# Kernel tuning notes

Hardware: AMD Instinct MI355X
Metric: run time of the kernel (lower is better)

The kernel has to match this reference:

```python
import jax, jax.numpy as jnp
import numpy as np

B, L, E, H = 4, 1024, 256, 8
DH = E // H  # head_size = 32


def setup_inputs() -> dict:
    key = jax.random.key(0)
    ks = jax.random.split(key, 12)
    node_features = jax.random.normal(ks[0], (B, L, E), dtype=jnp.float32)
    # sparse-ish adjacency with self loops so no row is all-masked
    adj = jax.random.bernoulli(ks[1], 0.05, (B, L, L))
    adj = adj | jnp.eye(L, dtype=bool)[None]
    key_edge_features = jax.random.normal(ks[2], (B, L, L, DH), dtype=jnp.float32)
    s = 1.0 / np.sqrt(E)
    Wq = jax.random.normal(ks[3], (E, E), dtype=jnp.float32) * s
    bq = jnp.zeros((E,), dtype=jnp.float32)
    Wk = jax.random.normal(ks[4], (E, E), dtype=jnp.float32) * s
    bk = jnp.zeros((E,), dtype=jnp.float32)
    Wv = jax.random.normal(ks[5], (E, E), dtype=jnp.float32) * s
    bv = jnp.zeros((E,), dtype=jnp.float32)
    Wo = jax.random.normal(ks[6], (E, E), dtype=jnp.float32) * s
    bo = jnp.zeros((E,), dtype=jnp.float32)
    return {"node_features": node_features, "batched_adj": adj,
            "key_edge_features": key_edge_features,
            "Wq": Wq, "bq": bq, "Wk": Wk, "bk": bk,
            "Wv": Wv, "bv": bv, "Wo": Wo, "bo": bo}


def _heads(x):
    # (B, L, E) -> (B, H, L, DH)
    b, l, _ = x.shape
    return x.reshape(b, l, H, DH).transpose(0, 2, 1, 3)


def reference(node_features, batched_adj, key_edge_features,
              Wq, bq, Wk, bk, Wv, bv, Wo, bo):
    Q = _heads(node_features @ Wq.T + bq)  # (B,H,L,DH)
    K = _heads(node_features @ Wk.T + bk)
    V = _heads(node_features @ Wv.T + bv)
    scores = jnp.einsum('bhnd,bhmd->bhnm', Q, K)
    scores = scores + jnp.einsum('bhnd,bnmd->bhnm', Q, key_edge_features)
    scores = scores / jnp.sqrt(jnp.asarray(E, dtype=scores.dtype))
    adj = batched_adj[:, None, :, :]  # (B,1,L,L) broadcast over heads
    scores = jnp.where(adj, scores, -jnp.inf)
    probs = jax.nn.softmax(scores, axis=-1)
    probs = jnp.where(jnp.isnan(probs), 0.0, probs)  # rows with no edges -> 0
    out = jnp.einsum('bhnm,bhmd->bhnd', probs, V)  # (B,H,L,DH)
    out = out.transpose(0, 2, 1, 3).reshape(node_features.shape[0], -1, E)
    return out @ Wo.T + bo
```

## Files before the change

### kernel.cpp

```cpp
#include <hip/hip_runtime.h>

#define Bv 4
#define Lv 1024
#define Ev 256
#define Hv 8
#define DHv 32

__global__ __launch_bounds__(256) void gemm_fused(
    const float* __restrict__ A,
    const float* __restrict__ W0, const float* __restrict__ b0, float* __restrict__ C0,
    const float* __restrict__ W1, const float* __restrict__ b1, float* __restrict__ C1,
    const float* __restrict__ W2, const float* __restrict__ b2, float* __restrict__ C2) {
    __shared__ float Xs[32][34];
    __shared__ float Ws[32][68];
    const int g = blockIdx.y >> 2;
    const float* __restrict__ W    = (g == 0) ? W0 : (g == 1) ? W1 : W2;
    const float* __restrict__ bias = (g == 0) ? b0 : (g == 1) ? b1 : b2;
    float* __restrict__ C          = (g == 0) ? C0 : (g == 1) ? C1 : C2;

    const int row0 = blockIdx.x * 32;
    const int col0 = (blockIdx.y & 3) * 64;
    const int t = threadIdx.x;
    const int tx = t & 15, ty = t >> 4;
    const int lr = t >> 3, lk = (t & 7) * 4;

    float acc[2][4] = {};

    for (int k0 = 0; k0 < 256; k0 += 32) {
        const float4 av = *(const float4*)&A[(size_t)(row0 + lr) * 256 + k0 + lk];
        const float4 w0 = *(const float4*)&W[(size_t)(col0 + lr) * 256 + k0 + lk];
        const float4 w1 = *(const float4*)&W[(size_t)(col0 + 32 + lr) * 256 + k0 + lk];
        Xs[lk + 0][lr] = av.x; Xs[lk + 1][lr] = av.y;
        Xs[lk + 2][lr] = av.z; Xs[lk + 3][lr] = av.w;
        Ws[lk + 0][lr] = w0.x; Ws[lk + 1][lr] = w0.y;
        Ws[lk + 2][lr] = w0.z; Ws[lk + 3][lr] = w0.w;
        Ws[lk + 0][32 + lr] = w1.x; Ws[lk + 1][32 + lr] = w1.y;
        Ws[lk + 2][32 + lr] = w1.z; Ws[lk + 3][32 + lr] = w1.w;
        __syncthreads();

        #pragma unroll
        for (int kk = 0; kk < 32; ++kk) {
            const float2 a2 = *(const float2*)&Xs[kk][ty * 2];
            const float4 b4 = *(const float4*)&Ws[kk][tx * 4];
            acc[0][0] = fmaf(a2.x, b4.x, acc[0][0]);
            acc[0][1] = fmaf(a2.x, b4.y, acc[0][1]);
            acc[0][2] = fmaf(a2.x, b4.z, acc[0][2]);
            acc[0][3] = fmaf(a2.x, b4.w, acc[0][3]);
            acc[1][0] = fmaf(a2.y, b4.x, acc[1][0]);
            acc[1][1] = fmaf(a2.y, b4.y, acc[1][1]);
            acc[1][2] = fmaf(a2.y, b4.z, acc[1][2]);
            acc[1][3] = fmaf(a2.y, b4.w, acc[1][3]);
        }
        __syncthreads();
    }

    const float4 bv4 = *(const float4*)&bias[col0 + tx * 4];
    #pragma unroll
    for (int ri = 0; ri < 2; ++ri) {
        const int row = row0 + ty * 2 + ri;
        float4 o;
        o.x = acc[ri][0] + bv4.x; o.y = acc[ri][1] + bv4.y;
        o.z = acc[ri][2] + bv4.z; o.w = acc[ri][3] + bv4.w;
        *(float4*)&C[(size_t)row * 256 + col0 + tx * 4] = o;
    }
}

__global__ __launch_bounds__(256) void attn_sparse(const float* __restrict__ Qb,
                                                   const float* __restrict__ Kb,
                                                   const float* __restrict__ Vb,
                                                   const int* __restrict__ adj,
                                                   const float* __restrict__ KE,
                                                   float* __restrict__ AT) {
    __shared__ __align__(16) float Qs[Ev];
    __shared__ __align__(16) float S[Hv][260];
    __shared__ int idxm[256];
    __shared__ int cntS;
    __shared__ float mh[Hv], lh[Hv], scaleh[Hv];

    const int bid = blockIdx.x;
    const int b = bid >> 10;
    const int n = bid & 1023;
    const int t = threadIdx.x;
    const int lane = t & 63;
    const int h_of_t = t >> 5;
    const size_t nrow = (size_t)(b * Lv + n) * Lv;

    Qs[t] = Qb[(size_t)(b * Lv + n) * Ev + t] * 0.0625f;
    if (t < Hv) { mh[t] = -1e30f; lh[t] = 0.f; }

    float acc = 0.f;
    const float* __restrict__ vcol = Vb + (size_t)b * Lv * Ev + t;
    const float4* __restrict__ K4 = (const float4*)Kb;
    const float4* __restrict__ KE4 = (const float4*)KE;
    const float4* __restrict__ Q4 = (const float4*)Qs;

    for (int c = 0; c < 4; ++c) {
        if (t == 0) cntS = 0;
        __syncthreads();

        const int m = c * 256 + t;
        const bool p = adj[nrow + m] != 0;
        const unsigned long long mask = __ballot(p);
        const int prefix = __popcll(mask & ((1ull << lane) - 1ull));
        int base = 0;
        if (lane == 0) base = atomicAdd(&cntS, __popcll(mask));
        base = __shfl(base, 0, 64);
        if (p) idxm[base + prefix] = m;
        __syncthreads();

        const int cnt = cntS;

        for (int tb = 0; tb < cnt * 8; tb += 256) {
            const int task = tb + t;
            if (task < cnt * 8) {
                const int ei = task >> 3, h = task & 7;
                const int mm = idxm[ei];
                const float4* kp = K4 + (size_t)(b * Lv + mm) * 64 + h * 8;
                const float4* kep = KE4 + (nrow + mm) * 8;
                const float4* qp = Q4 + h * 8;
                float dot = 0.f;
                #pragma unroll
                for (int j = 0; j < 8; ++j) {
                    const float4 kv = kp[j], kf = kep[j], qv = qp[j];
                    dot = fmaf(qv.x, kv.x + kf.x, dot);
                    dot = fmaf(qv.y, kv.y + kf.y, dot);
                    dot = fmaf(qv.z, kv.z + kf.z, dot);
                    dot = fmaf(qv.w, kv.w + kf.w, dot);
                }
                S[h][ei] = dot;
            }
        }
        __syncthreads();

        {
            const int h = t >> 5, d = t & 31;
            float cmax = -1e30f;
            for (int i = d; i < cnt; i += 32) cmax = fmaxf(cmax, S[h][i]);
            #pragma unroll
            for (int off = 16; off >= 1; off >>= 1)
                cmax = fmaxf(cmax, __shfl_xor(cmax, off, 64));
            const float oldm = mh[h];
            const float newm = fmaxf(oldm, cmax);
            float csum = 0.f;
            for (int i = d; i < cnt; i += 32) {
                const float pz = __expf(S[h][i] - newm);
                S[h][i] = pz;
                csum += pz;
            }
            #pragma unroll
            for (int off = 16; off >= 1; off >>= 1)
                csum += __shfl_xor(csum, off, 64);
            if (d == 0) {
                const float sc = __expf(oldm - newm);
                scaleh[h] = sc;
                lh[h] = lh[h] * sc + csum;
                mh[h] = newm;
            }
        }
        __syncthreads();

        {
            acc *= scaleh[h_of_t];
            int i = 0;
            for (; i + 4 <= cnt; i += 4) {
                const int m0 = idxm[i], m1 = idxm[i + 1], m2 = idxm[i + 2], m3 = idxm[i + 3];
                const float p0 = S[h_of_t][i],     p1 = S[h_of_t][i + 1];
                const float p2 = S[h_of_t][i + 2], p3 = S[h_of_t][i + 3];
                const float v0 = vcol[(size_t)m0 * Ev];
                const float v1 = vcol[(size_t)m1 * Ev];
                const float v2 = vcol[(size_t)m2 * Ev];
                const float v3 = vcol[(size_t)m3 * Ev];
                acc = fmaf(p0, v0, acc);
                acc = fmaf(p1, v1, acc);
                acc = fmaf(p2, v2, acc);
                acc = fmaf(p3, v3, acc);
            }
            for (; i < cnt; ++i)
                acc = fmaf(S[h_of_t][i], vcol[(size_t)idxm[i] * Ev], acc);
        }
        __syncthreads();
    }

    AT[(size_t)(b * Lv + n) * Ev + t] = acc / lh[h_of_t];
}

extern "C" void kernel_launch(void* const* d_in, const int* in_sizes, int n_in,
                              void* d_out, int out_size, void* d_ws, size_t ws_size,
                              hipStream_t stream) {
    const float* X   = (const float*)d_in[0];
    const int*   adj = (const int*)d_in[1];
    const float* KE  = (const float*)d_in[2];
    const float* Wq  = (const float*)d_in[3];
    const float* bq  = (const float*)d_in[4];
    const float* Wk  = (const float*)d_in[5];
    const float* bk  = (const float*)d_in[6];
    const float* Wv  = (const float*)d_in[7];
    const float* bv  = (const float*)d_in[8];
    const float* Wo  = (const float*)d_in[9];
    const float* bo  = (const float*)d_in[10];

    const size_t NE = (size_t)Bv * Lv * Ev;
    float* Qb = (float*)d_ws;
    float* Kb = Qb + NE;
    float* Vb = Kb + NE;
    float* AT = Vb + NE;
    float* out = (float*)d_out;

    const dim3 blk(256);

    hipLaunchKernelGGL(gemm_fused, dim3(128, 12), blk, 0, stream, X,
                       Wq, bq, Qb, Wk, bk, Kb, Wv, bv, Vb);
    hipLaunchKernelGGL(attn_sparse, dim3(Bv * Lv), blk, 0, stream,
                       Qb, Kb, Vb, adj, KE, AT);
    hipLaunchKernelGGL(gemm_fused, dim3(128, 4), blk, 0, stream, AT,
                       Wo, bo, out, Wo, bo, out, Wo, bo, out);
}
```

Before: 723.4 us.

## Compact adjacency once per row and enlarge GEMM tiles to 64x64

The attention kernel now compacts all four 256-column chunks of the adjacency row into one index list up front, then processes the nonzeros in chunks of 128. This replaces four chunk passes, each running a softmax update and several barriers, with roughly one or two passes at this sparsity. The projection GEMM tile grows from 32x64 to 64x64 with a 4x4 register micro-tile, which halves the block count and raises arithmetic per shared-memory load. In exchange the GEMM uses more registers and runs fewer blocks per launch.

```diff
diff --git a/kernel.cpp b/kernel.cpp
--- a/kernel.cpp
+++ b/kernel.cpp
@@ -5,59 +5,59 @@
 #define Ev 256
 #define Hv 8
 #define DHv 32
+#define CH 128
 
 __global__ __launch_bounds__(256) void gemm_fused(
     const float* __restrict__ A,
     const float* __restrict__ W0, const float* __restrict__ b0, float* __restrict__ C0,
     const float* __restrict__ W1, const float* __restrict__ b1, float* __restrict__ C1,
     const float* __restrict__ W2, const float* __restrict__ b2, float* __restrict__ C2) {
-    __shared__ float Xs[32][34];
+    __shared__ float Xs[32][68];
     __shared__ float Ws[32][68];
     const int g = blockIdx.y >> 2;
     const float* __restrict__ W    = (g == 0) ? W0 : (g == 1) ? W1 : W2;
     const float* __restrict__ bias = (g == 0) ? b0 : (g == 1) ? b1 : b2;
     float* __restrict__ C          = (g == 0) ? C0 : (g == 1) ? C1 : C2;
 
-    const int row0 = blockIdx.x * 32;
+    const int row0 = blockIdx.x * 64;
     const int col0 = (blockIdx.y & 3) * 64;
     const int t = threadIdx.x;
     const int tx = t & 15, ty = t >> 4;
-    const int lr = t >> 3, lk = (t & 7) * 4;
-
-    float acc[2][4] = {};
+    const int lr = t >> 2;
+    const int lk = (t & 3) * 8;
+
+    float acc[4][4] = {};
 
     for (int k0 = 0; k0 < 256; k0 += 32) {
-        const float4 av = *(const float4*)&A[(size_t)(row0 + lr) * 256 + k0 + lk];
+        const float4 a0 = *(const float4*)&A[(size_t)(row0 + lr) * 256 + k0 + lk];
+        const float4 a1 = *(const float4*)&A[(size_t)(row0 + lr) * 256 + k0 + lk + 4];
         const float4 w0 = *(const float4*)&W[(size_t)(col0 + lr) * 256 + k0 + lk];
-        const float4 w1 = *(const float4*)&W[(size_t)(col0 + 32 + lr) * 256 + k0 + lk];
-        Xs[lk + 0][lr] = av.x; Xs[lk + 1][lr] = av.y;
-        Xs[lk + 2][lr] = av.z; Xs[lk + 3][lr] = av.w;
-        Ws[lk + 0][lr] = w0.x; Ws[lk + 1][lr] = w0.y;
-        Ws[lk + 2][lr] = w0.z; Ws[lk + 3][lr] = w0.w;
-        Ws[lk + 0][32 + lr] = w1.x; Ws[lk + 1][32 + lr] = w1.y;
-        Ws[lk + 2][32 + lr] = w1.z; Ws[lk + 3][32 + lr] = w1.w;
+        const float4 w1 = *(const float4*)&W[(size_t)(col0 + lr) * 256 + k0 + lk + 4];
+        Xs[lk + 0][lr] = a0.x; Xs[lk + 1][lr] = a0.y; Xs[lk + 2][lr] = a0.z; Xs[lk + 3][lr] = a0.w;
+        Xs[lk + 4][lr] = a1.x; Xs[lk + 5][lr] = a1.y; Xs[lk + 6][lr] = a1.z; Xs[lk + 7][lr] = a1.w;
+        Ws[lk + 0][lr] = w0.x; Ws[lk + 1][lr] = w0.y; Ws[lk + 2][lr] = w0.z; Ws[lk + 3][lr] = w0.w;
+        Ws[lk + 4][lr] = w1.x; Ws[lk + 5][lr] = w1.y; Ws[lk + 6][lr] = w1.z; Ws[lk + 7][lr] = w1.w;
         __syncthreads();
 
         #pragma unroll
         for (int kk = 0; kk < 32; ++kk) {
-            const float2 a2 = *(const float2*)&Xs[kk][ty * 2];
+            const float4 a4 = *(const float4*)&Xs[kk][ty * 4];
             const float4 b4 = *(const float4*)&Ws[kk][tx * 4];
-            acc[0][0] = fmaf(a2.x, b4.x, acc[0][0]);
-            acc[0][1] = fmaf(a2.x, b4.y, acc[0][1]);
-            acc[0][2] = fmaf(a2.x, b4.z, acc[0][2]);
-            acc[0][3] = fmaf(a2.x, b4.w, acc[0][3]);
-            acc[1][0] = fmaf(a2.y, b4.x, acc[1][0]);
-            acc[1][1] = fmaf(a2.y, b4.y, acc[1][1]);
-            acc[1][2] = fmaf(a2.y, b4.z, acc[1][2]);
-            acc[1][3] = fmaf(a2.y, b4.w, acc[1][3]);
+            const float aa[4] = {a4.x, a4.y, a4.z, a4.w};
+            const float bb[4] = {b4.x, b4.y, b4.z, b4.w};
+            #pragma unroll
+            for (int ri = 0; ri < 4; ++ri)
+                #pragma unroll
+                for (int ci = 0; ci < 4; ++ci)
+                    acc[ri][ci] = fmaf(aa[ri], bb[ci], acc[ri][ci]);
         }
         __syncthreads();
     }
 
     const float4 bv4 = *(const float4*)&bias[col0 + tx * 4];
     #pragma unroll
-    for (int ri = 0; ri < 2; ++ri) {
-        const int row = row0 + ty * 2 + ri;
+    for (int ri = 0; ri < 4; ++ri) {
+        const int row = row0 + ty * 4 + ri;
         float4 o;
         o.x = acc[ri][0] + bv4.x; o.y = acc[ri][1] + bv4.y;
         o.z = acc[ri][2] + bv4.z; o.w = acc[ri][3] + bv4.w;
@@ -72,8 +72,8 @@
                                                    const float* __restrict__ KE,
                                                    float* __restrict__ AT) {
     __shared__ __align__(16) float Qs[Ev];
-    __shared__ __align__(16) float S[Hv][260];
-    __shared__ int idxm[256];
+    __shared__ int idxm[Lv];
+    __shared__ __align__(16) float S[Hv][CH + 4];
     __shared__ int cntS;
     __shared__ float mh[Hv], lh[Hv], scaleh[Hv];
 
@@ -82,67 +82,67 @@
     const int n = bid & 1023;
     const int t = threadIdx.x;
     const int lane = t & 63;
-    const int h_of_t = t >> 5;
+    const int h8 = t >> 5;
     const size_t nrow = (size_t)(b * Lv + n) * Lv;
 
     Qs[t] = Qb[(size_t)(b * Lv + n) * Ev + t] * 0.0625f;
+    if (t == 0) cntS = 0;
     if (t < Hv) { mh[t] = -1e30f; lh[t] = 0.f; }
-
+    __syncthreads();
+
+    #pragma unroll
+    for (int c = 0; c < 4; ++c) {
+        const int m = c * 256 + t;
+        const bool p = adj[nrow + m] != 0;
+        const unsigned long long mask = __ballot(p);
+        const int prefix = __popcll(mask & ((1ull << lane) - 1ull));
+        int base = 0;
+        if (lane == 0) base = atomicAdd(&cntS, (int)__popcll(mask));
+        base = __shfl(base, 0, 64);
+        if (p) idxm[base + prefix] = m;
+    }
+    __syncthreads();
+
+    const int cnt = cntS;
     float acc = 0.f;
     const float* __restrict__ vcol = Vb + (size_t)b * Lv * Ev + t;
     const float4* __restrict__ K4 = (const float4*)Kb;
     const float4* __restrict__ KE4 = (const float4*)KE;
     const float4* __restrict__ Q4 = (const float4*)Qs;
 
-    for (int c = 0; c < 4; ++c) {
-        if (t == 0) cntS = 0;
-        __syncthreads();
-
-        const int m = c * 256 + t;
-        const bool p = adj[nrow + m] != 0;
-        const unsigned long long mask = __ballot(p);
-        const int prefix = __popcll(mask & ((1ull << lane) - 1ull));
-        int base = 0;
-        if (lane == 0) base = atomicAdd(&cntS, __popcll(mask));
-        base = __shfl(base, 0, 64);
-        if (p) idxm[base + prefix] = m;
-        __syncthreads();
-
-        const int cnt = cntS;
-
-        for (int tb = 0; tb < cnt * 8; tb += 256) {
-            const int task = tb + t;
-            if (task < cnt * 8) {
-                const int ei = task >> 3, h = task & 7;
-                const int mm = idxm[ei];
-                const float4* kp = K4 + (size_t)(b * Lv + mm) * 64 + h * 8;
-                const float4* kep = KE4 + (nrow + mm) * 8;
-                const float4* qp = Q4 + h * 8;
-                float dot = 0.f;
-                #pragma unroll
-                for (int j = 0; j < 8; ++j) {
-                    const float4 kv = kp[j], kf = kep[j], qv = qp[j];
-                    dot = fmaf(qv.x, kv.x + kf.x, dot);
-                    dot = fmaf(qv.y, kv.y + kf.y, dot);
-                    dot = fmaf(qv.z, kv.z + kf.z, dot);
-                    dot = fmaf(qv.w, kv.w + kf.w, dot);
-                }
-                S[h][ei] = dot;
-            }
+    for (int eb = 0; eb < cnt; eb += CH) {
+        const int cc = min(CH, cnt - eb);
+
+        for (int task = t; task < cc * 8; task += 256) {
+            const int ei = task >> 3, h = task & 7;
+            const int mm = idxm[eb + ei];
+            const float4* kp = K4 + (size_t)(b * Lv + mm) * 64 + h * 8;
+            const float4* kep = KE4 + (nrow + mm) * 8;
+            const float4* qp = Q4 + h * 8;
+            float dot = 0.f;
+            #pragma unroll
+            for (int j = 0; j < 8; ++j) {
+                const float4 kv = kp[j], kf = kep[j], qv = qp[j];
+                dot = fmaf(qv.x, kv.x + kf.x, dot);
+                dot = fmaf(qv.y, kv.y + kf.y, dot);
+                dot = fmaf(qv.z, kv.z + kf.z, dot);
+                dot = fmaf(qv.w, kv.w + kf.w, dot);
+            }
+            S[h][ei] = dot;
         }
         __syncthreads();
 
         {
             const int h = t >> 5, d = t & 31;
             float cmax = -1e30f;
-            for (int i = d; i < cnt; i += 32) cmax = fmaxf(cmax, S[h][i]);
+            for (int i = d; i < cc; i += 32) cmax = fmaxf(cmax, S[h][i]);
             #pragma unroll
             for (int off = 16; off >= 1; off >>= 1)
                 cmax = fmaxf(cmax, __shfl_xor(cmax, off, 64));
             const float oldm = mh[h];
             const float newm = fmaxf(oldm, cmax);
             float csum = 0.f;
-            for (int i = d; i < cnt; i += 32) {
+            for (int i = d; i < cc; i += 32) {
                 const float pz = __expf(S[h][i] - newm);
                 S[h][i] = pz;
                 csum += pz;
@@ -159,13 +159,14 @@
         }
         __syncthreads();
 
+        acc *= scaleh[h8];
         {
-            acc *= scaleh[h_of_t];
             int i = 0;
-            for (; i + 4 <= cnt; i += 4) {
-                const int m0 = idxm[i], m1 = idxm[i + 1], m2 = idxm[i + 2], m3 = idxm[i + 3];
-                const float p0 = S[h_of_t][i],     p1 = S[h_of_t][i + 1];
-                const float p2 = S[h_of_t][i + 2], p3 = S[h_of_t][i + 3];
+            for (; i + 4 <= cc; i += 4) {
+                const int m0 = idxm[eb + i],     m1 = idxm[eb + i + 1];
+                const int m2 = idxm[eb + i + 2], m3 = idxm[eb + i + 3];
+                const float p0 = S[h8][i],     p1 = S[h8][i + 1];
+                const float p2 = S[h8][i + 2], p3 = S[h8][i + 3];
                 const float v0 = vcol[(size_t)m0 * Ev];
                 const float v1 = vcol[(size_t)m1 * Ev];
                 const float v2 = vcol[(size_t)m2 * Ev];
@@ -175,13 +176,13 @@
                 acc = fmaf(p2, v2, acc);
                 acc = fmaf(p3, v3, acc);
             }
-            for (; i < cnt; ++i)
-                acc = fmaf(S[h_of_t][i], vcol[(size_t)idxm[i] * Ev], acc);
-        }
-        __syncthreads();
-    }
-
-    AT[(size_t)(b * Lv + n) * Ev + t] = acc / lh[h_of_t];
+            for (; i < cc; ++i)
+                acc = fmaf(S[h8][i], vcol[(size_t)idxm[eb + i] * Ev], acc);
+        }
+        __syncthreads();
+    }
+
+    AT[(size_t)(b * Lv + n) * Ev + t] = acc / lh[h8];
 }
 
 extern "C" void kernel_launch(void* const* d_in, const int* in_sizes, int n_in,
@@ -208,10 +209,10 @@
 
     const dim3 blk(256);
 
-    hipLaunchKernelGGL(gemm_fused, dim3(128, 12), blk, 0, stream, X,
+    hipLaunchKernelGGL(gemm_fused, dim3(64, 12), blk, 0, stream, X,
                        Wq, bq, Qb, Wk, bk, Kb, Wv, bv, Vb);
     hipLaunchKernelGGL(attn_sparse, dim3(Bv * Lv), blk, 0, stream,
                        Qb, Kb, Vb, adj, KE, AT);
-    hipLaunchKernelGGL(gemm_fused, dim3(128, 4), blk, 0, stream, AT,
+    hipLaunchKernelGGL(gemm_fused, dim3(64, 4), blk, 0, stream, AT,
                        Wo, bo, out, Wo, bo, out, Wo, bo, out);
 }
```

Result: slower. 745.2 us (+3.0%).
